# Kernel tuning notes

Hardware: AMD Instinct MI355X
Metric: run time of the kernel (lower is better)

## Reference

```python
import jax, jax.numpy as jnp
import numpy as np

B, QN, D_IN = 2, 2048, 1024
NDS = QN // 2
HEADS, DIM_HEAD = 16, 64
INNER = HEADS * DIM_HEAD  # 1024
D_OUT = 1024


def setup_inputs() -> dict:
    key = jax.random.key(0)
    ks = jax.random.split(key, 7)
    s = 0.02
    return {
        "unet_full": jax.random.normal(ks[0], (B, QN, D_IN), jnp.float32),
        "unet_downsampled": jax.random.normal(ks[1], (B, NDS, D_IN), jnp.float32),
        "Wq": jax.random.normal(ks[2], (D_IN, INNER), jnp.float32) * s,
        "Wk": jax.random.normal(ks[3], (D_IN, INNER), jnp.float32) * s,
        "Wv": jax.random.normal(ks[4], (D_IN, INNER), jnp.float32) * s,
        "Wo": jax.random.normal(ks[5], (INNER, D_OUT), jnp.float32) * s,
        "bo": jnp.zeros((D_OUT,), jnp.float32),
    }


def reference(unet_full, unet_downsampled, Wq, Wk, Wv, Wo, bo):
    # projections
    q = unet_full @ Wq                      # [B, QN, H*D]
    k = unet_downsampled @ Wk               # [B, NDS, H*D]
    v = unet_downsampled @ Wv
    # repeat kv along sequence dim (torch repeat(1,2,1) == tile twice on dim 1)
    k = jnp.concatenate([k, k], axis=1)     # [B, KVN=2*NDS, H*D]
    v = jnp.concatenate([v, v], axis=1)
    kvn = k.shape[1]
    # split heads
    q = q.reshape(B, QN, HEADS, DIM_HEAD)
    k = k.reshape(B, kvn, HEADS, DIM_HEAD)
    v = v.reshape(B, kvn, HEADS, DIM_HEAD)
    # banded mask: triu(diagonal=-2) keeps entries where j >= i - 2; log -> 0 allowed, -inf blocked
    i = jnp.arange(QN)[:, None]
    j = jnp.arange(kvn)[None, :]
    bias = jnp.where(j >= i - 2, 0.0, -jnp.inf).astype(q.dtype)  # [QN, KVN]
    scale = 1.0 / jnp.sqrt(jnp.asarray(DIM_HEAD, q.dtype))
    scores = jnp.einsum('bqhd,bkhd->bhqk', q, k) * scale + bias[None, None]
    attn = jax.nn.softmax(scores, axis=-1)
    out = jnp.einsum('bhqk,bkhd->bqhd', attn, v)  # [B, QN, H, D]
    out = out.reshape(B, QN, INNER)
    return out @ Wo + bo
```

## Files before the change

kernel.cpp:

```cpp
#include <hip/hip_runtime.h>

typedef __attribute__((ext_vector_type(8))) short short8;
typedef __attribute__((ext_vector_type(4))) short short4v;
typedef __attribute__((ext_vector_type(4))) float floatx4;
typedef __attribute__((ext_vector_type(4))) unsigned int uint4v;
typedef __attribute__((ext_vector_type(2))) unsigned int uint2v;

__device__ __forceinline__ unsigned short f2bf(float f) {
  unsigned u = __float_as_uint(f);
  u += 0x7FFFu + ((u >> 16) & 1u);
  return (unsigned short)(u >> 16);
}
__device__ __forceinline__ unsigned pack_bf2(float f0, float f1) {
  unsigned a = __float_as_uint(f0) + 0x8000u;
  unsigned b = __float_as_uint(f1) + 0x8000u;
  return __builtin_amdgcn_perm(b, a, 0x07060302u);
}
__device__ __forceinline__ void async16(const unsigned short* g, unsigned short* l) {
  __builtin_amdgcn_global_load_lds(
      (const __attribute__((address_space(1))) unsigned int*)g,
      (__attribute__((address_space(3))) unsigned int*)l, 16, 0, 0);
}

#define B_   2
#define QN_  2048
#define NDS_ 1024
#define H_   16
#define C_SC 0.18033688011f

__global__ __launch_bounds__(256) void prep(
    const float* __restrict__ Wq, const float* __restrict__ Wk,
    const float* __restrict__ Wv, const float* __restrict__ Wo,
    unsigned short* __restrict__ WT) {
  int bid = blockIdx.x;
  int z = bid >> 8, tile = bid & 255;
  const float* W = z == 0 ? Wq : z == 1 ? Wk : z == 2 ? Wv : Wo;
  unsigned short* out = WT + (size_t)z * (1u << 20);
  __shared__ unsigned short tilebuf[64][65];
  int bi = tile >> 4, bj = tile & 15;
  int c = threadIdx.x & 63, r0 = threadIdx.x >> 6;
#pragma unroll
  for (int i = 0; i < 64; i += 4)
    tilebuf[r0 + i][c] = f2bf(W[(size_t)(bi * 64 + r0 + i) * 1024 + bj * 64 + c]);
  __syncthreads();
#pragma unroll
  for (int i = 0; i < 64; i += 4)
    out[(size_t)(bj * 64 + r0 + i) * 1024 + bi * 64 + c] = tilebuf[c][r0 + i];
}

__global__ __launch_bounds__(512) void gemm_qkv(
    const float* __restrict__ full, const float* __restrict__ ds,
    const unsigned short* __restrict__ WT,
    unsigned short* __restrict__ Qb, unsigned short* __restrict__ Kb,
    unsigned short* __restrict__ Vt) {
  __shared__ __align__(16) unsigned short As[128 * 64];
  __shared__ __align__(16) unsigned short Bs[128 * 64];
  int t = threadIdx.x;
  int lane = t & 63, wave = t >> 6;
  int lrow = lane & 15, quad = lane >> 4;
  int by = blockIdx.x;
  int colBase = blockIdx.y * 128;
  int wr = (wave & 3) * 32, wc = (wave >> 2) * 64;
  int sw = lrow & 7;

  int sel = (by < 32) ? 0 : (by < 48 ? 1 : 2);
  const unsigned short* Wt = WT + (size_t)sel * (1u << 20);
  const float* Afp = (sel == 0) ? full : ds;
  size_t arow0 = (sel == 0) ? (size_t)by * 128
                            : (size_t)(by - (sel == 1 ? 32 : 48)) * 128;

  floatx4 acc[2][4];
#pragma unroll
  for (int mi = 0; mi < 2; ++mi)
#pragma unroll
    for (int ni = 0; ni < 4; ++ni) acc[mi][ni] = (floatx4){0.f, 0.f, 0.f, 0.f};

  for (int k0 = 0; k0 < 1024; k0 += 64) {
    __syncthreads();
#pragma unroll
    for (int it = 0; it < 2; ++it) {
      int linear = it * 512 + t;
      int row = linear >> 3;
      int cg = (linear & 7) ^ (row & 7);
      const float* p = Afp + (arow0 + row) * 1024 + k0 + cg * 8;
      floatx4 x = *(const floatx4*)p, y = *(const floatx4*)(p + 4);
      uint4v u = {pack_bf2(x[0], x[1]), pack_bf2(x[2], x[3]),
                  pack_bf2(y[0], y[1]), pack_bf2(y[2], y[3])};
      *(uint4v*)&As[linear * 8] = u;
      async16(Wt + (size_t)(colBase + row) * 1024 + k0 + cg * 8, Bs + linear * 8);
    }
    __syncthreads();

#pragma unroll
    for (int ks = 0; ks < 2; ++ks) {
      int fc = ((ks * 4 + quad) ^ sw) * 8;
      short8 af[2], bfr[4];
#pragma unroll
      for (int mi = 0; mi < 2; ++mi)
        af[mi] = *(const short8*)&As[(wr + mi * 16 + lrow) * 64 + fc];
#pragma unroll
      for (int ni = 0; ni < 4; ++ni)
        bfr[ni] = *(const short8*)&Bs[(wc + ni * 16 + lrow) * 64 + fc];
#pragma unroll
      for (int mi = 0; mi < 2; ++mi)
#pragma unroll
        for (int ni = 0; ni < 4; ++ni)
          acc[mi][ni] =
              __builtin_amdgcn_mfma_f32_16x16x32_bf16(af[mi], bfr[ni], acc[mi][ni], 0, 0, 0);
    }
  }

#pragma unroll
  for (int mi = 0; mi < 2; ++mi)
#pragma unroll
    for (int ni = 0; ni < 4; ++ni) {
      int col = colBase + wc + ni * 16 + lrow;
      if (sel == 2) {
        size_t r0g = arow0 + wr + mi * 16 + quad * 4;
        size_t b = r0g >> 10, kv = r0g & 1023;
        short4v pk;
#pragma unroll
        for (int r = 0; r < 4; ++r) pk[r] = (short)f2bf(acc[mi][ni][r]);
        *(short4v*)&Vt[b * (1u << 20) + (size_t)col * 1024 + kv] = pk;
      } else {
        unsigned short* C = (sel == 0) ? Qb : Kb;
#pragma unroll
        for (int r = 0; r < 4; ++r) {
          size_t row = arow0 + wr + mi * 16 + quad * 4 + r;
          C[row * 1024 + col] = f2bf(acc[mi][ni][r]);
        }
      }
    }
}

#define PSTR 40
__global__ __launch_bounds__(512) void attn_kernel(
    const unsigned short* __restrict__ Q,
    const unsigned short* __restrict__ K,
    const unsigned short* __restrict__ V,
    unsigned short* __restrict__ O) {
  __shared__ __align__(16) unsigned short Ks[2][32 * 64];
  __shared__ __align__(16) unsigned short Vs[2][64 * 32];
  __shared__ __align__(16) unsigned short Pl[8][16 * PSTR];
  int t = threadIdx.x, lane = t & 63, wave = t >> 6;
  int lrow = lane & 15, quad = lane >> 4;
  int bh = blockIdx.y, b = bh >> 4, h = bh & 15;
  int q0 = blockIdx.x * 128, qtile = q0 + wave * 16;
  int swk = lrow & 7, swv = (lrow >> 1) & 3;

  const unsigned short* qp =
      Q + (size_t)(b * QN_ + qtile + lrow) * 1024 + h * 64 + quad * 8;
  short8 qb0 = *(const short8*)qp;
  short8 qb1 = *(const short8*)(qp + 32);

  int ts = t & 255;
  int krow = ts >> 3, kq = (ts & 7) ^ (krow & 7);
  const unsigned short* ksrc =
      K + (size_t)(b * NDS_ + krow) * 1024 + h * 64 + kq * 8;
  int vrow = ts >> 2, vq = (ts & 3) ^ ((vrow >> 1) & 3);
  const unsigned short* vsrc =
      V + ((size_t)b * 1024 + h * 64 + vrow) * 1024 + vq * 8;

  int c0 = (q0 >= 1058) ? (((q0 - 1058) >> 5) + 1) : 0;
  if (t < 256) async16(ksrc + (size_t)c0 * 32 * 1024, &Ks[0][ts * 8]);
  else         async16(vsrc + c0 * 32, &Vs[0][ts * 8]);
  const unsigned short* kpre = ksrc + (size_t)(c0 + 1) * 32 * 1024;
  const unsigned short* vpre = vsrc + (c0 + 1) * 32;

  floatx4 acc_o[4];
#pragma unroll
  for (int dt = 0; dt < 4; ++dt) acc_o[dt] = (floatx4){0.f, 0.f, 0.f, 0.f};
  float den0 = 0.f, den1 = 0.f;
  int t1 = qtile + lrow - 2, t2 = qtile + lrow - 1026;
  unsigned short* P = Pl[wave];
  int buf = 0;

  for (int c = c0; c < 32; ++c) {
    __syncthreads();
    if (c + 1 < 32) {
      if (t < 256) async16(kpre, &Ks[buf ^ 1][ts * 8]);
      else         async16(vpre, &Vs[buf ^ 1][ts * 8]);
      kpre += 32 * 1024;
      vpre += 32;
    }
    int cb = c * 32;
    if (cb + 31 >= qtile - 1026) {
      bool fast2 = (cb >= qtile + 13);
      bool fast1 = (cb <= qtile - 34) && (cb >= qtile - 1011);
      if (fast1 || fast2) {
        float bias = fast2 ? 1.f : 0.f;
#pragma unroll
        for (int nt = 0; nt < 2; ++nt) {
          const unsigned short* kb = &Ks[buf][(nt * 16 + lrow) * 64];
          short8 ka0 = *(const short8*)(kb + (quad ^ swk) * 8);
          short8 ka1 = *(const short8*)(kb + ((quad + 4) ^ swk) * 8);
          __builtin_amdgcn_s_setprio(1);
          floatx4 z = (floatx4){0.f, 0.f, 0.f, 0.f};
          z = __builtin_amdgcn_mfma_f32_16x16x32_bf16(ka0, qb0, z, 0, 0, 0);
          z = __builtin_amdgcn_mfma_f32_16x16x32_bf16(ka1, qb1, z, 0, 0, 0);
          __builtin_amdgcn_s_setprio(0);
          float p[4];
#pragma unroll
          for (int r = 0; r < 4; ++r) {
            p[r] = __builtin_amdgcn_exp2f(fmaf(z[r], C_SC, bias));
            if (nt == 0) den0 += p[r]; else den1 += p[r];
          }
          uint2v pw = {pack_bf2(p[0], p[1]), pack_bf2(p[2], p[3])};
          *(uint2v*)&P[lrow * PSTR + nt * 16 + quad * 4] = pw;
        }
      } else {
#pragma unroll
        for (int nt = 0; nt < 2; ++nt) {
          const unsigned short* kb = &Ks[buf][(nt * 16 + lrow) * 64];
          short8 ka0 = *(const short8*)(kb + (quad ^ swk) * 8);
          short8 ka1 = *(const short8*)(kb + ((quad + 4) ^ swk) * 8);
          __builtin_amdgcn_s_setprio(1);
          floatx4 z = (floatx4){0.f, 0.f, 0.f, 0.f};
          z = __builtin_amdgcn_mfma_f32_16x16x32_bf16(ka0, qb0, z, 0, 0, 0);
          z = __builtin_amdgcn_mfma_f32_16x16x32_bf16(ka1, qb1, z, 0, 0, 0);
          __builtin_amdgcn_s_setprio(0);
          float p[4];
#pragma unroll
          for (int r = 0; r < 4; ++r) {
            int j0 = cb + nt * 16 + quad * 4 + r;
            float m = (j0 >= t1 ? 1.f : 0.f) + (j0 >= t2 ? 1.f : 0.f);
            p[r] = m * __builtin_amdgcn_exp2f(z[r] * C_SC);
            if (nt == 0) den0 += p[r]; else den1 += p[r];
          }
          uint2v pw = {pack_bf2(p[0], p[1]), pack_bf2(p[2], p[3])};
          *(uint2v*)&P[lrow * PSTR + nt * 16 + quad * 4] = pw;
        }
      }
      short8 pa = *(const short8*)&P[lrow * PSTR + quad * 8];
      __builtin_amdgcn_s_setprio(1);
#pragma unroll
      for (int dt = 0; dt < 4; ++dt) {
        short8 vf =
            *(const short8*)&Vs[buf][(dt * 16 + lrow) * 32 + (quad ^ swv) * 8];
        acc_o[dt] = __builtin_amdgcn_mfma_f32_16x16x32_bf16(pa, vf, acc_o[dt], 0, 0, 0);
      }
      __builtin_amdgcn_s_setprio(0);
    }
    buf ^= 1;
  }
  float denom = den0 + den1;
  denom += __shfl_xor(denom, 16);
  denom += __shfl_xor(denom, 32);
  float dd[4];
#pragma unroll
  for (int r = 0; r < 4; ++r) dd[r] = __shfl(denom, quad * 4 + r);
#pragma unroll
  for (int dt = 0; dt < 4; ++dt)
#pragma unroll
    for (int r = 0; r < 4; ++r) {
      int i = qtile + quad * 4 + r;
      int col = h * 64 + dt * 16 + lrow;
      O[(size_t)(b * QN_ + i) * 1024 + col] = f2bf(acc_o[dt][r] / dd[r]);
    }
}

__global__ __launch_bounds__(512) void gemm_o(
    const unsigned short* __restrict__ Ab, const unsigned short* __restrict__ WoT,
    const float* __restrict__ bo, float* __restrict__ out) {
  __shared__ __align__(16) unsigned short As[64 * 64];
  __shared__ __align__(16) unsigned short Bs[128 * 64];
  int t = threadIdx.x;
  int lane = t & 63, wave = t >> 6;
  int lrow = lane & 15, quad = lane >> 4;
  size_t rowBase = (size_t)blockIdx.x * 64;
  int colBase = blockIdx.y * 128;
  int wr = (wave & 1) * 32, wc = (wave >> 1) * 32;
  int sw = lrow & 7;

  floatx4 acc[2][2];
#pragma unroll
  for (int mi = 0; mi < 2; ++mi)
#pragma unroll
    for (int ni = 0; ni < 2; ++ni) acc[mi][ni] = (floatx4){0.f, 0.f, 0.f, 0.f};

  for (int k0 = 0; k0 < 1024; k0 += 64) {
    __syncthreads();
    {
      int row = t >> 3;
      int cg = (t & 7) ^ (row & 7);
      async16(Ab + (rowBase + row) * 1024 + k0 + cg * 8, As + t * 8);
    }
#pragma unroll
    for (int it = 0; it < 2; ++it) {
      int linear = it * 512 + t;
      int row = linear >> 3;
      int cg = (linear & 7) ^ (row & 7);
      async16(WoT + (size_t)(colBase + row) * 1024 + k0 + cg * 8, Bs + linear * 8);
    }
    __syncthreads();

#pragma unroll
    for (int ks = 0; ks < 2; ++ks) {
      int fc = ((ks * 4 + quad) ^ sw) * 8;
      short8 af[2], bfr[2];
#pragma unroll
      for (int mi = 0; mi < 2; ++mi)
        af[mi] = *(const short8*)&As[(wr + mi * 16 + lrow) * 64 + fc];
#pragma unroll
      for (int ni = 0; ni < 2; ++ni)
        bfr[ni] = *(const short8*)&Bs[(wc + ni * 16 + lrow) * 64 + fc];
#pragma unroll
      for (int mi = 0; mi < 2; ++mi)
#pragma unroll
        for (int ni = 0; ni < 2; ++ni)
          acc[mi][ni] =
              __builtin_amdgcn_mfma_f32_16x16x32_bf16(af[mi], bfr[ni], acc[mi][ni], 0, 0, 0);
    }
  }

#pragma unroll
  for (int mi = 0; mi < 2; ++mi)
#pragma unroll
    for (int ni = 0; ni < 2; ++ni) {
      int col = colBase + wc + ni * 16 + lrow;
      float badd = bo[col];
#pragma unroll
      for (int r = 0; r < 4; ++r) {
        size_t row = rowBase + wr + mi * 16 + quad * 4 + r;
        out[row * 1024 + col] = acc[mi][ni][r] + badd;
      }
    }
}

extern "C" void kernel_launch(void* const* d_in, const int* in_sizes, int n_in,
                              void* d_out, int out_size, void* d_ws, size_t ws_size,
                              hipStream_t stream) {
  const float* full = (const float*)d_in[0];
  const float* ds   = (const float*)d_in[1];
  const float* Wq   = (const float*)d_in[2];
  const float* Wk   = (const float*)d_in[3];
  const float* Wv   = (const float*)d_in[4];
  const float* Wo   = (const float*)d_in[5];
  const float* bo   = (const float*)d_in[6];
  float* out = (float*)d_out;

  unsigned short* ws = (unsigned short*)d_ws;
  unsigned short* Qb  = ws;
  unsigned short* Kb  = ws + (4u << 20);
  unsigned short* Vt  = ws + (6u << 20);
  unsigned short* Ab  = ws + (8u << 20);
  unsigned short* WT  = ws + (12u << 20);
  unsigned short* WoT = WT + 3u * (1u << 20);

  prep<<<1024, 256, 0, stream>>>(Wq, Wk, Wv, Wo, WT);
  gemm_qkv<<<dim3(64, 8), 512, 0, stream>>>(full, ds, WT, Qb, Kb, Vt);
  attn_kernel<<<dim3(QN_ / 128, B_ * H_), 512, 0, stream>>>(Qb, Kb, Vt, Ab);
  gemm_o<<<dim3(64, 8), 512, 0, stream>>>(Ab, WoT, bo, out);
}
```

Before: 163.0 us.

## Keep softmax probabilities in registers by permuting V's kv layout

The attention kernel no longer sends P through LDS between the QK^T and PV MFMAs. Each lane packs its own probabilities straight into the A operand, and the kv dimension of V is stored permuted by the QKV GEMM epilogue so the MFMA k-ordering still lines up. This removes an LDS write/read round trip per tile and the Pl shared buffer, which may also help occupancy. Separately, the weight transpose/convert prep kernel now writes 8-byte vectors instead of 2-byte stores.

```diff
diff --git a/kernel.cpp b/kernel.cpp
--- a/kernel.cpp
+++ b/kernel.cpp
@@ -43,9 +43,15 @@
   for (int i = 0; i < 64; i += 4)
     tilebuf[r0 + i][c] = f2bf(W[(size_t)(bi * 64 + r0 + i) * 1024 + bj * 64 + c]);
   __syncthreads();
-#pragma unroll
-  for (int i = 0; i < 64; i += 4)
-    out[(size_t)(bj * 64 + r0 + i) * 1024 + bi * 64 + c] = tilebuf[c][r0 + i];
+  int c4 = (threadIdx.x & 15) * 4, rr = threadIdx.x >> 4;
+#pragma unroll
+  for (int i = 0; i < 64; i += 16) {
+    int r = rr + i;
+    short4v v;
+#pragma unroll
+    for (int j = 0; j < 4; ++j) v[j] = (short)tilebuf[c4 + j][r];
+    *(short4v*)&out[(size_t)(bj * 64 + r) * 1024 + bi * 64 + c4] = v;
+  }
 }
 
 __global__ __launch_bounds__(512) void gemm_qkv(
@@ -118,10 +124,14 @@
       if (sel == 2) {
         size_t r0g = arow0 + wr + mi * 16 + quad * 4;
         size_t b = r0g >> 10, kv = r0g & 1023;
+        int p = (int)(kv & 31);
+        int a = p >> 2;
+        int lg = (a < 4) ? (a << 3) : (((a - 4) << 3) | 4);
+        size_t kvp = (kv & ~(size_t)31) | (size_t)lg;
         short4v pk;
 #pragma unroll
         for (int r = 0; r < 4; ++r) pk[r] = (short)f2bf(acc[mi][ni][r]);
-        *(short4v*)&Vt[b * (1u << 20) + (size_t)col * 1024 + kv] = pk;
+        *(short4v*)&Vt[b * (1u << 20) + (size_t)col * 1024 + kvp] = pk;
       } else {
         unsigned short* C = (sel == 0) ? Qb : Kb;
 #pragma unroll
@@ -133,7 +143,6 @@
     }
 }
 
-#define PSTR 40
 __global__ __launch_bounds__(512) void attn_kernel(
     const unsigned short* __restrict__ Q,
     const unsigned short* __restrict__ K,
@@ -141,7 +150,6 @@
     unsigned short* __restrict__ O) {
   __shared__ __align__(16) unsigned short Ks[2][32 * 64];
   __shared__ __align__(16) unsigned short Vs[2][64 * 32];
-  __shared__ __align__(16) unsigned short Pl[8][16 * PSTR];
   int t = threadIdx.x, lane = t & 63, wave = t >> 6;
   int lrow = lane & 15, quad = lane >> 4;
   int bh = blockIdx.y, b = bh >> 4, h = bh & 15;
@@ -172,7 +180,6 @@
   for (int dt = 0; dt < 4; ++dt) acc_o[dt] = (floatx4){0.f, 0.f, 0.f, 0.f};
   float den0 = 0.f, den1 = 0.f;
   int t1 = qtile + lrow - 2, t2 = qtile + lrow - 1026;
-  unsigned short* P = Pl[wave];
   int buf = 0;
 
   for (int c = c0; c < 32; ++c) {
@@ -185,6 +192,7 @@
     }
     int cb = c * 32;
     if (cb + 31 >= qtile - 1026) {
+      unsigned pk0, pk1, pk2, pk3;
       bool fast2 = (cb >= qtile + 13);
       bool fast1 = (cb <= qtile - 34) && (cb >= qtile - 1011);
       if (fast1 || fast2) {
@@ -205,8 +213,8 @@
             p[r] = __builtin_amdgcn_exp2f(fmaf(z[r], C_SC, bias));
             if (nt == 0) den0 += p[r]; else den1 += p[r];
           }
-          uint2v pw = {pack_bf2(p[0], p[1]), pack_bf2(p[2], p[3])};
-          *(uint2v*)&P[lrow * PSTR + nt * 16 + quad * 4] = pw;
+          if (nt == 0) { pk0 = pack_bf2(p[0], p[1]); pk1 = pack_bf2(p[2], p[3]); }
+          else         { pk2 = pack_bf2(p[0], p[1]); pk3 = pack_bf2(p[2], p[3]); }
         }
       } else {
 #pragma unroll
@@ -227,11 +235,15 @@
             p[r] = m * __builtin_amdgcn_exp2f(z[r] * C_SC);
             if (nt == 0) den0 += p[r]; else den1 += p[r];
           }
-          uint2v pw = {pack_bf2(p[0], p[1]), pack_bf2(p[2], p[3])};
-          *(uint2v*)&P[lrow * PSTR + nt * 16 + quad * 4] = pw;
+          if (nt == 0) { pk0 = pack_bf2(p[0], p[1]); pk1 = pack_bf2(p[2], p[3]); }
+          else         { pk2 = pack_bf2(p[0], p[1]); pk3 = pack_bf2(p[2], p[3]); }
         }
       }
-      short8 pa = *(const short8*)&P[lrow * PSTR + quad * 8];
+      short8 pa;
+      {
+        uint4v u = {pk0, pk1, pk2, pk3};
+        __builtin_memcpy(&pa, &u, 16);
+      }
       __builtin_amdgcn_s_setprio(1);
 #pragma unroll
       for (int dt = 0; dt < 4; ++dt) {
```

Measured after the change: 155.8 us (median of 2 runs). 1.05x faster.
